# Kernel tuning notes

Hardware: AMD Instinct MI355X
Metric: run time of the kernel (lower is better)

Reference implementation:

```python
import jax, jax.numpy as jnp
import numpy as np

B, C, D, H, W = 8, 1, 128, 160, 128

def setup_inputs() -> dict:
    key = jax.random.key(0)
    kx, kb = jax.random.split(key)
    x = jax.random.normal(kx, (B, C, D, H, W), dtype=jnp.float32)
    base_volume = jax.random.normal(kb, (C, D, H, W), dtype=jnp.float32)
    return {"x": x, "base_volume": base_volume}

def reference(x, base_volume):
    # skimage match_histograms for continuous float images reduces (for a.e.-unique
    # values) to: map each source voxel's empirical CDF quantile onto the template's
    # inverse CDF via linear interpolation.
    tmpl = base_volume.ravel()
    t_sorted = jnp.sort(tmpl)                      # template inverse-CDF values
    M = tmpl.shape[0]
    tq = jnp.arange(1, M + 1, dtype=x.dtype) / M   # template CDF quantiles

    def match_one(sample):
        flat = sample.ravel()
        N = flat.shape[0]
        # rank of each voxel within its own sample (double argsort)
        ranks = jnp.argsort(jnp.argsort(flat))
        q = (ranks + 1).astype(flat.dtype) / N     # source empirical CDF
        matched = jnp.interp(q, tq, t_sorted)
        return matched.reshape(sample.shape)

    matched_vol = jax.vmap(match_one)(x)
    # self.model is identity here (the kernel headroom is the matching itself)
    return matched_vol
```

## Files before the change

kernel.cpp:

```cpp
#include <hip/hip_runtime.h>
#include <stdint.h>


#define SEG_N 2621440
#define NSEG 9
#define TILE 4096
#define NBLK (SEG_N / TILE)
#define RADIX 256
#define HL (RADIX * NBLK)
#define SCHUNK 4096
#define SNB (HL / SCHUNK)
#define SBUF (TILE + (TILE >> 4))

__device__ __forceinline__ uint32_t fkey(float f) {
  uint32_t b = __float_as_uint(f);
  return b ^ ((b & 0x80000000u) ? 0xFFFFFFFFu : 0x80000000u);
}
__device__ __forceinline__ float finv(uint32_t u) {
  uint32_t b = u ^ ((u & 0x80000000u) ? 0x80000000u : 0xFFFFFFFFu);
  return __uint_as_float(b);
}
__device__ __forceinline__ uint32_t SIDX(uint32_t i) { return i + (i >> 4); }

__global__ __launch_bounds__(256) void init_k(const float* __restrict__ x,
                                              const float* __restrict__ tmpl,
                                              int segbase,
                                              uint64_t* __restrict__ pairsA,
                                              uint32_t* __restrict__ Hkb) {
  __shared__ uint32_t hist[RADIX];
  const int t = threadIdx.x;
  const int blk = blockIdx.x;
  const int sl = blockIdx.y;
  const int seg = segbase + sl;
  const float* src = (seg == 0) ? tmpl : (x + (size_t)(seg - 1) * SEG_N);
  uint64_t* pa = pairsA + (size_t)sl * SEG_N;
  hist[t] = 0;
  __syncthreads();
  const uint32_t base = blk * TILE;
  const float4* s4 = reinterpret_cast<const float4*>(src + base);
#pragma unroll
  for (int r = 0; r < 4; ++r) {
    float4 v = s4[r * 256 + t];
    uint32_t i0 = base + (uint32_t)(r * 256 + t) * 4u;
    float f[4] = {v.x, v.y, v.z, v.w};
#pragma unroll
    for (int c = 0; c < 4; ++c) {
      uint32_t k = fkey(f[c]);
      atomicAdd(&hist[k & 255u], 1u);
      pa[i0 + c] = ((uint64_t)k << 32) | (uint64_t)(i0 + c);
    }
  }
  __syncthreads();
  Hkb[(size_t)sl * HL + (size_t)blk * RADIX + t] = hist[t];
}

__global__ __launch_bounds__(256) void hist_k(const uint64_t* __restrict__ pairs,
                                              uint32_t* __restrict__ Hkb, int p) {
  __shared__ uint32_t hist[RADIX];
  const int t = threadIdx.x;
  const int blk = blockIdx.x;
  const int sl = blockIdx.y;
  const uint64_t* pc = pairs + (size_t)sl * SEG_N + (size_t)blk * TILE;
  hist[t] = 0;
  __syncthreads();
  const int sh = 32 + 8 * p;
#pragma unroll
  for (int r = 0; r < 16; ++r) {
    uint64_t e = pc[r * 256 + t];
    atomicAdd(&hist[(uint32_t)(e >> sh) & 255u], 1u);
  }
  __syncthreads();
  Hkb[(size_t)sl * HL + (size_t)blk * RADIX + t] = hist[t];
}

__global__ __launch_bounds__(256) void transp_k(const uint32_t* __restrict__ Hkb,
                                                uint32_t* __restrict__ Hbk) {
  __shared__ uint32_t tile[64][65];
  const int sl = blockIdx.y;
  const uint32_t* src = Hkb + (size_t)sl * HL;
  uint32_t* dst = Hbk + (size_t)sl * HL;
  const int kt = blockIdx.x % (NBLK / 64);
  const int bt = blockIdx.x / (NBLK / 64);
  const int tx = threadIdx.x & 63, ty = threadIdx.x >> 6;
#pragma unroll
  for (int r = 0; r < 16; ++r) {
    int k = kt * 64 + ty + r * 4;
    tile[ty + r * 4][tx] = src[(size_t)k * RADIX + bt * 64 + tx];
  }
  __syncthreads();
#pragma unroll
  for (int r = 0; r < 16; ++r) {
    int b = bt * 64 + ty + r * 4;
    dst[(size_t)b * NBLK + kt * 64 + tx] = tile[tx][ty + r * 4];
  }
}

__device__ __forceinline__ uint32_t block_excl_scan_256(uint32_t v, uint32_t* lds) {
  const int t = threadIdx.x;
  lds[t] = v;
  __syncthreads();
#pragma unroll
  for (int off = 1; off < 256; off <<= 1) {
    uint32_t a = (t >= off) ? lds[t - off] : 0u;
    __syncthreads();
    lds[t] += a;
    __syncthreads();
  }
  uint32_t ex = (t == 0) ? 0u : lds[t - 1];
  __syncthreads();
  return ex;
}

__global__ __launch_bounds__(256) void scan_a_k(const uint32_t* __restrict__ Hbk,
                                                uint32_t* __restrict__ partials) {
  __shared__ uint32_t lds[256];
  const int t = threadIdx.x;
  const uint32_t* c = Hbk + (size_t)blockIdx.y * HL +
                      (size_t)blockIdx.x * SCHUNK + (size_t)t * 16;
  const uint4* p = reinterpret_cast<const uint4*>(c);
  uint32_t s = 0;
#pragma unroll
  for (int k = 0; k < 4; ++k) { uint4 a = p[k]; s += a.x + a.y + a.z + a.w; }
  lds[t] = s;
  __syncthreads();
  for (int off = 128; off > 0; off >>= 1) {
    if (t < off) lds[t] += lds[t + off];
    __syncthreads();
  }
  if (t == 0) partials[blockIdx.y * 64 + blockIdx.x] = lds[0];
}

__global__ __launch_bounds__(256) void scan_b_k(uint32_t* __restrict__ partials) {
  __shared__ uint32_t lds[256];
  const int t = threadIdx.x;
  uint32_t* p = partials + blockIdx.y * 64;
  uint32_t v = (t < SNB) ? p[t] : 0u;
  uint32_t ex = block_excl_scan_256(v, lds);
  if (t < SNB) p[t] = ex;
}

__global__ __launch_bounds__(256) void scan_c_k(uint32_t* __restrict__ Hbk,
                                                const uint32_t* __restrict__ partials) {
  __shared__ uint32_t lds[256];
  const int t = threadIdx.x;
  uint32_t* c = Hbk + (size_t)blockIdx.y * HL +
                (size_t)blockIdx.x * SCHUNK + (size_t)t * 16;
  uint4* p = reinterpret_cast<uint4*>(c);
  uint4 a[4];
  uint32_t s = 0;
#pragma unroll
  for (int k = 0; k < 4; ++k) {
    a[k] = p[k];
    s += a[k].x + a[k].y + a[k].z + a[k].w;
  }
  uint32_t ex = block_excl_scan_256(s, lds);
  uint32_t run = partials[blockIdx.y * 64 + blockIdx.x] + ex;
#pragma unroll
  for (int k = 0; k < 4; ++k) {
    uint4 o;
    o.x = run; run += a[k].x;
    o.y = run; run += a[k].y;
    o.z = run; run += a[k].z;
    o.w = run; run += a[k].w;
    p[k] = o;
  }
}

__device__ __forceinline__ void scan_pack2(uint32_t v0, uint32_t v1, uint32_t* s,
                                           uint32_t& ex0, uint32_t& ex1,
                                           uint32_t& tot0, uint32_t& tot1) {
  const int lane = threadIdx.x & 63, w = threadIdx.x >> 6;
  uint32_t a = v0, b = v1;
#pragma unroll
  for (int o = 1; o < 64; o <<= 1) {
    uint32_t na = __shfl_up(a, (unsigned)o, 64);
    uint32_t nb = __shfl_up(b, (unsigned)o, 64);
    if (lane >= o) { a += na; b += nb; }
  }
  if (lane == 63) { s[w] = a; s[4 + w] = b; }
  __syncthreads();
  if (threadIdx.x == 0) {
    uint32_t r0 = 0, r1 = 0;
#pragma unroll
    for (int i = 0; i < 4; ++i) {
      uint32_t q0 = s[i], q1 = s[4 + i];
      s[i] = r0; s[4 + i] = r1;
      r0 += q0; r1 += q1;
    }
    s[8] = r0; s[9] = r1;
  }
  __syncthreads();
  ex0 = a - v0 + s[w];
  ex1 = b - v1 + s[4 + w];
  tot0 = s[8]; tot1 = s[9];
  __syncthreads();
}

template <int P, int MODE>
__global__ __launch_bounds__(256) void part_k(const uint64_t* __restrict__ src,
                                              uint64_t* __restrict__ dst,
                                              const uint32_t* __restrict__ Hbk,
                                              float* __restrict__ tsorted,
                                              float* __restrict__ out,
                                              int segbase, int slbase) {
  __shared__ uint64_t buf[SBUF];
  __shared__ uint32_t ldsStart[RADIX];
  __shared__ uint32_t ldsBase[RADIX];
  __shared__ uint32_t scanS[12];
  const int t = threadIdx.x;
  const int blk = blockIdx.x;
  const int sl = slbase + blockIdx.y;
  const int seg = segbase + sl;
  const uint64_t* ps = src + (size_t)sl * SEG_N + (size_t)blk * TILE;

  ldsBase[t] = Hbk[(size_t)sl * HL + (size_t)t * NBLK + blk];

#pragma unroll
  for (int r = 0; r < 16; ++r) buf[SIDX(r * 256 + t)] = ps[r * 256 + t];
  __syncthreads();

  uint64_t e[16];
#pragma unroll
  for (int rnd = 0; rnd < 4; ++rnd) {
#pragma unroll
    for (int j = 0; j < 16; ++j) e[j] = buf[SIDX(t * 16 + j)];
    uint32_t cnt[4] = {0u, 0u, 0u, 0u};
#pragma unroll
    for (int j = 0; j < 16; ++j) {
      uint32_t d2 = (uint32_t)(e[j] >> (32 + 8 * P + 2 * rnd)) & 3u;
      cnt[d2]++;
    }
    uint32_t p0 = cnt[0] | (cnt[1] << 16);
    uint32_t p1 = cnt[2] | (cnt[3] << 16);
    uint32_t ex0, ex1, tot0, tot1;
    scan_pack2(p0, p1, scanS, ex0, ex1, tot0, tot1);
    uint32_t t0 = tot0 & 0xffffu, t1 = tot0 >> 16, t2 = tot1 & 0xffffu;
    uint32_t pos[4];
    pos[0] = (ex0 & 0xffffu);
    pos[1] = t0 + (ex0 >> 16);
    pos[2] = t0 + t1 + (ex1 & 0xffffu);
    pos[3] = t0 + t1 + t2 + (ex1 >> 16);
#pragma unroll
    for (int j = 0; j < 16; ++j) {
      uint32_t d2 = (uint32_t)(e[j] >> (32 + 8 * P + 2 * rnd)) & 3u;
      buf[SIDX(pos[d2]++)] = e[j];
    }
    __syncthreads();
  }

  const uint8_t* b8 = reinterpret_cast<const uint8_t*>(buf);
#pragma unroll
  for (int r = 0; r < 16; ++r) {
    uint32_t s = (uint32_t)(r * 256 + t);
    e[r] = buf[SIDX(s)];
    uint32_t d = (uint32_t)(e[r] >> (32 + 8 * P)) & 255u;
    uint32_t dp = (s == 0) ? 0x100u
                           : (uint32_t)b8[(size_t)SIDX(s - 1) * 8 + 4 + P];
    if (d != dp) ldsStart[d] = s;
  }
  __syncthreads();

#pragma unroll
  for (int r = 0; r < 16; ++r) {
    uint32_t s = (uint32_t)(r * 256 + t);
    uint64_t el = e[r];
    uint32_t d = (uint32_t)(el >> (32 + 8 * P)) & 255u;
    uint32_t dest = ldsBase[d] + s - ldsStart[d];
    if (MODE == 0) {
      dst[(size_t)sl * SEG_N + dest] = el;
    } else if (MODE == 1) {
      tsorted[dest] = finv((uint32_t)(el >> 32));
    } else {
      out[(size_t)(seg - 1) * SEG_N + (uint32_t)el] = tsorted[dest];
    }
  }
}

extern "C" void kernel_launch(void* const* d_in, const int* in_sizes, int n_in,
                              void* d_out, int out_size, void* d_ws, size_t ws_size,
                              hipStream_t stream) {
  const float* x = (const float*)d_in[0];
  const float* tmpl = (const float*)d_in[1];
  float* out = (float*)d_out;

  auto need = [](int nb) -> size_t {
    return (size_t)nb * ((size_t)SEG_N * 16 + (size_t)HL * 8 + 256) +
           (size_t)SEG_N * 4 + 8192;
  };
  const int nb = (ws_size >= need(9)) ? 9 : (ws_size >= need(3)) ? 3 : 1;

  uint8_t* w = (uint8_t*)d_ws;
  size_t off = 0;
  auto carve = [&](size_t bytes) -> void* {
    void* p = w + off;
    off = (off + bytes + 255) & ~(size_t)255;
    return p;
  };
  uint64_t* pairsA = (uint64_t*)carve((size_t)nb * SEG_N * 8);
  uint64_t* pairsB = (uint64_t*)carve((size_t)nb * SEG_N * 8);
  uint32_t* Hkb = (uint32_t*)carve((size_t)nb * HL * 4);
  uint32_t* Hbk = (uint32_t*)carve((size_t)nb * HL * 4);
  uint32_t* partials = (uint32_t*)carve((size_t)nb * 64 * 4);
  float* tsorted = (float*)carve((size_t)SEG_N * 4);

  for (int g = 0; g < NSEG; g += nb) {
    const dim3 gi(NBLK, nb);
    const dim3 gt(40, nb);
    const dim3 gs(SNB, nb);
    const dim3 g1(1, nb);

    auto scan_h = [&]() {
      transp_k<<<gt, 256, 0, stream>>>(Hkb, Hbk);
      scan_a_k<<<gs, 256, 0, stream>>>(Hbk, partials);
      scan_b_k<<<g1, 256, 0, stream>>>(partials);
      scan_c_k<<<gs, 256, 0, stream>>>(Hbk, partials);
    };

    init_k<<<gi, 256, 0, stream>>>(x, tmpl, g, pairsA, Hkb);
    scan_h();
    part_k<0, 0><<<gi, 256, 0, stream>>>(pairsA, pairsB, Hbk, tsorted, out, g, 0);
    hist_k<<<gi, 256, 0, stream>>>(pairsB, Hkb, 1);
    scan_h();
    part_k<1, 0><<<gi, 256, 0, stream>>>(pairsB, pairsA, Hbk, tsorted, out, g, 0);
    hist_k<<<gi, 256, 0, stream>>>(pairsA, Hkb, 2);
    scan_h();
    part_k<2, 0><<<gi, 256, 0, stream>>>(pairsA, pairsB, Hbk, tsorted, out, g, 0);
    hist_k<<<gi, 256, 0, stream>>>(pairsB, Hkb, 3);
    scan_h();
    if (g == 0) {
      part_k<3, 1><<<dim3(NBLK, 1), 256, 0, stream>>>(pairsB, pairsA, Hbk,
                                                      tsorted, out, g, 0);
      if (nb > 1)
        part_k<3, 2><<<dim3(NBLK, nb - 1), 256, 0, stream>>>(pairsB, pairsA, Hbk,
                                                             tsorted, out, g, 1);
    } else {
      part_k<3, 2><<<dim3(NBLK, nb), 256, 0, stream>>>(pairsB, pairsA, Hbk,
                                                       tsorted, out, g, 0);
    }
  }
}
```

Before: 1.133 ms.

## Fuse next-pass histogram into radix scatter via global atomics, drop hist and transpose

```diff
diff --git a/kernel.cpp b/kernel.cpp
--- a/kernel.cpp
+++ b/kernel.cpp
@@ -54,25 +54,6 @@
   Hkb[(size_t)sl * HL + (size_t)blk * RADIX + t] = hist[t];
 }
 
-__global__ __launch_bounds__(256) void hist_k(const uint64_t* __restrict__ pairs,
-                                              uint32_t* __restrict__ Hkb, int p) {
-  __shared__ uint32_t hist[RADIX];
-  const int t = threadIdx.x;
-  const int blk = blockIdx.x;
-  const int sl = blockIdx.y;
-  const uint64_t* pc = pairs + (size_t)sl * SEG_N + (size_t)blk * TILE;
-  hist[t] = 0;
-  __syncthreads();
-  const int sh = 32 + 8 * p;
-#pragma unroll
-  for (int r = 0; r < 16; ++r) {
-    uint64_t e = pc[r * 256 + t];
-    atomicAdd(&hist[(uint32_t)(e >> sh) & 255u], 1u);
-  }
-  __syncthreads();
-  Hkb[(size_t)sl * HL + (size_t)blk * RADIX + t] = hist[t];
-}
-
 __global__ __launch_bounds__(256) void transp_k(const uint32_t* __restrict__ Hkb,
                                                 uint32_t* __restrict__ Hbk) {
   __shared__ uint32_t tile[64][65];
@@ -111,16 +92,23 @@
   return ex;
 }
 
-__global__ __launch_bounds__(256) void scan_a_k(const uint32_t* __restrict__ Hbk,
-                                                uint32_t* __restrict__ partials) {
+__global__ __launch_bounds__(256) void scan_a_k(const uint32_t* __restrict__ cnt,
+                                                uint32_t* __restrict__ partials,
+                                                uint32_t* __restrict__ zbuf) {
   __shared__ uint32_t lds[256];
   const int t = threadIdx.x;
-  const uint32_t* c = Hbk + (size_t)blockIdx.y * HL +
-                      (size_t)blockIdx.x * SCHUNK + (size_t)t * 16;
-  const uint4* p = reinterpret_cast<const uint4*>(c);
+  const size_t boff = (size_t)blockIdx.y * HL + (size_t)blockIdx.x * SCHUNK +
+                      (size_t)t * 16;
+  const uint4* p = reinterpret_cast<const uint4*>(cnt + boff);
   uint32_t s = 0;
 #pragma unroll
   for (int k = 0; k < 4; ++k) { uint4 a = p[k]; s += a.x + a.y + a.z + a.w; }
+  if (zbuf) {
+    uint4* q = reinterpret_cast<uint4*>(zbuf + boff);
+    uint4 z = {0u, 0u, 0u, 0u};
+#pragma unroll
+    for (int k = 0; k < 4; ++k) q[k] = z;
+  }
   lds[t] = s;
   __syncthreads();
   for (int off = 128; off > 0; off >>= 1) {
@@ -139,11 +127,11 @@
   if (t < SNB) p[t] = ex;
 }
 
-__global__ __launch_bounds__(256) void scan_c_k(uint32_t* __restrict__ Hbk,
+__global__ __launch_bounds__(256) void scan_c_k(uint32_t* __restrict__ cnt,
                                                 const uint32_t* __restrict__ partials) {
   __shared__ uint32_t lds[256];
   const int t = threadIdx.x;
-  uint32_t* c = Hbk + (size_t)blockIdx.y * HL +
+  uint32_t* c = cnt + (size_t)blockIdx.y * HL +
                 (size_t)blockIdx.x * SCHUNK + (size_t)t * 16;
   uint4* p = reinterpret_cast<uint4*>(c);
   uint4 a[4];
@@ -196,10 +184,11 @@
   __syncthreads();
 }
 
-template <int P, int MODE>
+template <int P, int MODE, int ACC>
 __global__ __launch_bounds__(256) void part_k(const uint64_t* __restrict__ src,
                                               uint64_t* __restrict__ dst,
                                               const uint32_t* __restrict__ Hbk,
+                                              uint32_t* __restrict__ HbkN,
                                               float* __restrict__ tsorted,
                                               float* __restrict__ out,
                                               int segbase, int slbase) {
@@ -264,14 +253,19 @@
   for (int r = 0; r < 16; ++r) {
     uint32_t s = (uint32_t)(r * 256 + t);
     uint64_t el = e[r];
-    uint32_t d = (uint32_t)(el >> (32 + 8 * P)) & 255u;
+    uint32_t key = (uint32_t)(el >> 32);
+    uint32_t d = (key >> (8 * P)) & 255u;
     uint32_t dest = ldsBase[d] + s - ldsStart[d];
     if (MODE == 0) {
       dst[(size_t)sl * SEG_N + dest] = el;
     } else if (MODE == 1) {
-      tsorted[dest] = finv((uint32_t)(el >> 32));
+      tsorted[dest] = finv(key);
     } else {
       out[(size_t)(seg - 1) * SEG_N + (uint32_t)el] = tsorted[dest];
+    }
+    if (ACC) {
+      uint32_t nd = (key >> (8 * (P + 1 < 4 ? P + 1 : 0))) & 255u;
+      atomicAdd(&HbkN[(size_t)sl * HL + (size_t)nd * NBLK + (dest >> 12)], 1u);
     }
   }
 }
@@ -309,33 +303,34 @@
     const dim3 gs(SNB, nb);
     const dim3 g1(1, nb);
 
-    auto scan_h = [&]() {
-      transp_k<<<gt, 256, 0, stream>>>(Hkb, Hbk);
-      scan_a_k<<<gs, 256, 0, stream>>>(Hbk, partials);
+    auto scan_h = [&](uint32_t* cur, uint32_t* zb) {
+      scan_a_k<<<gs, 256, 0, stream>>>(cur, partials, zb);
       scan_b_k<<<g1, 256, 0, stream>>>(partials);
-      scan_c_k<<<gs, 256, 0, stream>>>(Hbk, partials);
+      scan_c_k<<<gs, 256, 0, stream>>>(cur, partials);
     };
 
     init_k<<<gi, 256, 0, stream>>>(x, tmpl, g, pairsA, Hkb);
-    scan_h();
-    part_k<0, 0><<<gi, 256, 0, stream>>>(pairsA, pairsB, Hbk, tsorted, out, g, 0);
-    hist_k<<<gi, 256, 0, stream>>>(pairsB, Hkb, 1);
-    scan_h();
-    part_k<1, 0><<<gi, 256, 0, stream>>>(pairsB, pairsA, Hbk, tsorted, out, g, 0);
-    hist_k<<<gi, 256, 0, stream>>>(pairsA, Hkb, 2);
-    scan_h();
-    part_k<2, 0><<<gi, 256, 0, stream>>>(pairsA, pairsB, Hbk, tsorted, out, g, 0);
-    hist_k<<<gi, 256, 0, stream>>>(pairsB, Hkb, 3);
-    scan_h();
+    transp_k<<<gt, 256, 0, stream>>>(Hkb, Hbk);
+    scan_h(Hbk, Hkb);
+    part_k<0, 0, 1><<<gi, 256, 0, stream>>>(pairsA, pairsB, Hbk, Hkb,
+                                            tsorted, out, g, 0);
+    scan_h(Hkb, Hbk);
+    part_k<1, 0, 1><<<gi, 256, 0, stream>>>(pairsB, pairsA, Hkb, Hbk,
+                                            tsorted, out, g, 0);
+    scan_h(Hbk, Hkb);
+    part_k<2, 0, 1><<<gi, 256, 0, stream>>>(pairsA, pairsB, Hbk, Hkb,
+                                            tsorted, out, g, 0);
+    scan_h(Hkb, nullptr);
     if (g == 0) {
-      part_k<3, 1><<<dim3(NBLK, 1), 256, 0, stream>>>(pairsB, pairsA, Hbk,
-                                                      tsorted, out, g, 0);
+      part_k<3, 1, 0><<<dim3(NBLK, 1), 256, 0, stream>>>(pairsB, pairsA, Hkb,
+                                                         nullptr, tsorted, out,
+                                                         g, 0);
       if (nb > 1)
-        part_k<3, 2><<<dim3(NBLK, nb - 1), 256, 0, stream>>>(pairsB, pairsA, Hbk,
-                                                             tsorted, out, g, 1);
+        part_k<3, 2, 0><<<dim3(NBLK, nb - 1), 256, 0, stream>>>(
+            pairsB, pairsA, Hkb, nullptr, tsorted, out, g, 1);
     } else {
-      part_k<3, 2><<<dim3(NBLK, nb), 256, 0, stream>>>(pairsB, pairsA, Hbk,
-                                                       tsorted, out, g, 0);
-    }
-  }
-}
+      part_k<3, 2, 0><<<dim3(NBLK, nb), 256, 0, stream>>>(
+          pairsB, pairsA, Hkb, nullptr, tsorted, out, g, 0);
+    }
+  }
+}
```

Result: slower. 4.457 ms (+293.3%).

## Split radix-sort key/index pairs into separate arrays and skip template indices

Applied to the files above, without the earlier changes.

```diff
diff --git a/kernel.cpp b/kernel.cpp
--- a/kernel.cpp
+++ b/kernel.cpp
@@ -10,7 +10,7 @@
 #define HL (RADIX * NBLK)
 #define SCHUNK 4096
 #define SNB (HL / SCHUNK)
-#define SBUF (TILE + (TILE >> 4))
+#define SBUFE (TILE + (TILE >> 4))
 
 __device__ __forceinline__ uint32_t fkey(float f) {
   uint32_t b = __float_as_uint(f);
@@ -25,52 +25,66 @@
 __global__ __launch_bounds__(256) void init_k(const float* __restrict__ x,
                                               const float* __restrict__ tmpl,
                                               int segbase,
-                                              uint64_t* __restrict__ pairsA,
+                                              uint32_t* __restrict__ keyA,
+                                              uint32_t* __restrict__ idxA,
                                               uint32_t* __restrict__ Hkb) {
-  __shared__ uint32_t hist[RADIX];
+  __shared__ uint32_t hw[4 * RADIX];
   const int t = threadIdx.x;
   const int blk = blockIdx.x;
   const int sl = blockIdx.y;
   const int seg = segbase + sl;
   const float* src = (seg == 0) ? tmpl : (x + (size_t)(seg - 1) * SEG_N);
-  uint64_t* pa = pairsA + (size_t)sl * SEG_N;
-  hist[t] = 0;
-  __syncthreads();
+  uint32_t* ka = keyA + (size_t)sl * SEG_N;
+  uint32_t* ia = idxA + (size_t)sl * SEG_N;
+  hw[t] = 0; hw[t + 256] = 0; hw[t + 512] = 0; hw[t + 768] = 0;
+  __syncthreads();
+  const int w = t >> 6;
   const uint32_t base = blk * TILE;
   const float4* s4 = reinterpret_cast<const float4*>(src + base);
 #pragma unroll
   for (int r = 0; r < 4; ++r) {
     float4 v = s4[r * 256 + t];
     uint32_t i0 = base + (uint32_t)(r * 256 + t) * 4u;
-    float f[4] = {v.x, v.y, v.z, v.w};
-#pragma unroll
-    for (int c = 0; c < 4; ++c) {
-      uint32_t k = fkey(f[c]);
-      atomicAdd(&hist[k & 255u], 1u);
-      pa[i0 + c] = ((uint64_t)k << 32) | (uint64_t)(i0 + c);
-    }
-  }
-  __syncthreads();
-  Hkb[(size_t)sl * HL + (size_t)blk * RADIX + t] = hist[t];
-}
-
-__global__ __launch_bounds__(256) void hist_k(const uint64_t* __restrict__ pairs,
+    uint4 kv;
+    kv.x = fkey(v.x); kv.y = fkey(v.y); kv.z = fkey(v.z); kv.w = fkey(v.w);
+    atomicAdd(&hw[w * 256 + (kv.x & 255u)], 1u);
+    atomicAdd(&hw[w * 256 + (kv.y & 255u)], 1u);
+    atomicAdd(&hw[w * 256 + (kv.z & 255u)], 1u);
+    atomicAdd(&hw[w * 256 + (kv.w & 255u)], 1u);
+    *reinterpret_cast<uint4*>(ka + i0) = kv;
+    if (seg != 0) {
+      uint4 iv = {i0, i0 + 1u, i0 + 2u, i0 + 3u};
+      *reinterpret_cast<uint4*>(ia + i0) = iv;
+    }
+  }
+  __syncthreads();
+  Hkb[(size_t)sl * HL + (size_t)blk * RADIX + t] =
+      hw[t] + hw[t + 256] + hw[t + 512] + hw[t + 768];
+}
+
+__global__ __launch_bounds__(256) void hist_k(const uint32_t* __restrict__ keys,
                                               uint32_t* __restrict__ Hkb, int p) {
-  __shared__ uint32_t hist[RADIX];
+  __shared__ uint32_t hw[4 * RADIX];
   const int t = threadIdx.x;
   const int blk = blockIdx.x;
   const int sl = blockIdx.y;
-  const uint64_t* pc = pairs + (size_t)sl * SEG_N + (size_t)blk * TILE;
-  hist[t] = 0;
-  __syncthreads();
-  const int sh = 32 + 8 * p;
-#pragma unroll
-  for (int r = 0; r < 16; ++r) {
-    uint64_t e = pc[r * 256 + t];
-    atomicAdd(&hist[(uint32_t)(e >> sh) & 255u], 1u);
-  }
-  __syncthreads();
-  Hkb[(size_t)sl * HL + (size_t)blk * RADIX + t] = hist[t];
+  const uint32_t* kc = keys + (size_t)sl * SEG_N + (size_t)blk * TILE;
+  hw[t] = 0; hw[t + 256] = 0; hw[t + 512] = 0; hw[t + 768] = 0;
+  __syncthreads();
+  const int w = t >> 6;
+  const int sh = 8 * p;
+  const uint4* k4 = reinterpret_cast<const uint4*>(kc);
+#pragma unroll
+  for (int r = 0; r < 4; ++r) {
+    uint4 v = k4[r * 256 + t];
+    atomicAdd(&hw[w * 256 + ((v.x >> sh) & 255u)], 1u);
+    atomicAdd(&hw[w * 256 + ((v.y >> sh) & 255u)], 1u);
+    atomicAdd(&hw[w * 256 + ((v.z >> sh) & 255u)], 1u);
+    atomicAdd(&hw[w * 256 + ((v.w >> sh) & 255u)], 1u);
+  }
+  __syncthreads();
+  Hkb[(size_t)sl * HL + (size_t)blk * RADIX + t] =
+      hw[t] + hw[t + 256] + hw[t + 512] + hw[t + 768];
 }
 
 __global__ __launch_bounds__(256) void transp_k(const uint32_t* __restrict__ Hkb,
@@ -197,13 +211,16 @@
 }
 
 template <int P, int MODE>
-__global__ __launch_bounds__(256) void part_k(const uint64_t* __restrict__ src,
-                                              uint64_t* __restrict__ dst,
+__global__ __launch_bounds__(256) void part_k(const uint32_t* __restrict__ keyIn,
+                                              const uint32_t* __restrict__ idxIn,
+                                              uint32_t* __restrict__ keyOut,
+                                              uint32_t* __restrict__ idxOut,
                                               const uint32_t* __restrict__ Hbk,
                                               float* __restrict__ tsorted,
                                               float* __restrict__ out,
                                               int segbase, int slbase) {
-  __shared__ uint64_t buf[SBUF];
+  __shared__ uint32_t bufK[SBUFE];
+  __shared__ uint16_t bufP[SBUFE];
   __shared__ uint32_t ldsStart[RADIX];
   __shared__ uint32_t ldsBase[RADIX];
   __shared__ uint32_t scanS[12];
@@ -211,23 +228,34 @@
   const int blk = blockIdx.x;
   const int sl = slbase + blockIdx.y;
   const int seg = segbase + sl;
-  const uint64_t* ps = src + (size_t)sl * SEG_N + (size_t)blk * TILE;
+  const bool wantIdx = (seg != 0);
+  const size_t segOff = (size_t)sl * SEG_N;
+  const uint32_t blkBase = (uint32_t)blk * TILE;
+  const uint32_t* ks = keyIn + segOff + blkBase;
 
   ldsBase[t] = Hbk[(size_t)sl * HL + (size_t)t * NBLK + blk];
 
 #pragma unroll
-  for (int r = 0; r < 16; ++r) buf[SIDX(r * 256 + t)] = ps[r * 256 + t];
-  __syncthreads();
-
-  uint64_t e[16];
+  for (int r = 0; r < 16; ++r) {
+    uint32_t s = (uint32_t)(r * 256 + t);
+    bufK[SIDX(s)] = ks[s];
+    bufP[SIDX(s)] = (uint16_t)s;
+  }
+  __syncthreads();
+
+  uint32_t k[16];
+  uint16_t pr[16];
 #pragma unroll
   for (int rnd = 0; rnd < 4; ++rnd) {
 #pragma unroll
-    for (int j = 0; j < 16; ++j) e[j] = buf[SIDX(t * 16 + j)];
+    for (int j = 0; j < 16; ++j) {
+      k[j] = bufK[SIDX(t * 16 + j)];
+      pr[j] = bufP[SIDX(t * 16 + j)];
+    }
     uint32_t cnt[4] = {0u, 0u, 0u, 0u};
 #pragma unroll
     for (int j = 0; j < 16; ++j) {
-      uint32_t d2 = (uint32_t)(e[j] >> (32 + 8 * P + 2 * rnd)) & 3u;
+      uint32_t d2 = (k[j] >> (8 * P + 2 * rnd)) & 3u;
       cnt[d2]++;
     }
     uint32_t p0 = cnt[0] | (cnt[1] << 16);
@@ -242,20 +270,23 @@
     pos[3] = t0 + t1 + t2 + (ex1 >> 16);
 #pragma unroll
     for (int j = 0; j < 16; ++j) {
-      uint32_t d2 = (uint32_t)(e[j] >> (32 + 8 * P + 2 * rnd)) & 3u;
-      buf[SIDX(pos[d2]++)] = e[j];
+      uint32_t d2 = (k[j] >> (8 * P + 2 * rnd)) & 3u;
+      uint32_t pp = pos[d2]++;
+      bufK[SIDX(pp)] = k[j];
+      bufP[SIDX(pp)] = pr[j];
     }
     __syncthreads();
   }
 
-  const uint8_t* b8 = reinterpret_cast<const uint8_t*>(buf);
+  const uint8_t* b8 = reinterpret_cast<const uint8_t*>(bufK);
 #pragma unroll
   for (int r = 0; r < 16; ++r) {
     uint32_t s = (uint32_t)(r * 256 + t);
-    e[r] = buf[SIDX(s)];
-    uint32_t d = (uint32_t)(e[r] >> (32 + 8 * P)) & 255u;
+    k[r] = bufK[SIDX(s)];
+    pr[r] = bufP[SIDX(s)];
+    uint32_t d = (k[r] >> (8 * P)) & 255u;
     uint32_t dp = (s == 0) ? 0x100u
-                           : (uint32_t)b8[(size_t)SIDX(s - 1) * 8 + 4 + P];
+                           : (uint32_t)b8[(size_t)SIDX(s - 1) * 4 + P];
     if (d != dp) ldsStart[d] = s;
   }
   __syncthreads();
@@ -263,15 +294,17 @@
 #pragma unroll
   for (int r = 0; r < 16; ++r) {
     uint32_t s = (uint32_t)(r * 256 + t);
-    uint64_t el = e[r];
-    uint32_t d = (uint32_t)(el >> (32 + 8 * P)) & 255u;
+    uint32_t key = k[r];
+    uint32_t d = (key >> (8 * P)) & 255u;
     uint32_t dest = ldsBase[d] + s - ldsStart[d];
     if (MODE == 0) {
-      dst[(size_t)sl * SEG_N + dest] = el;
+      keyOut[segOff + dest] = key;
+      if (wantIdx) idxOut[segOff + dest] = idxIn[segOff + blkBase + pr[r]];
     } else if (MODE == 1) {
-      tsorted[dest] = finv((uint32_t)(el >> 32));
+      tsorted[dest] = finv(key);
     } else {
-      out[(size_t)(seg - 1) * SEG_N + (uint32_t)el] = tsorted[dest];
+      uint32_t gidx = idxIn[segOff + blkBase + pr[r]];
+      out[(size_t)(seg - 1) * SEG_N + gidx] = tsorted[dest];
     }
   }
 }
@@ -296,8 +329,10 @@
     off = (off + bytes + 255) & ~(size_t)255;
     return p;
   };
-  uint64_t* pairsA = (uint64_t*)carve((size_t)nb * SEG_N * 8);
-  uint64_t* pairsB = (uint64_t*)carve((size_t)nb * SEG_N * 8);
+  uint32_t* keyA = (uint32_t*)carve((size_t)nb * SEG_N * 4);
+  uint32_t* keyB = (uint32_t*)carve((size_t)nb * SEG_N * 4);
+  uint32_t* idxA = (uint32_t*)carve((size_t)nb * SEG_N * 4);
+  uint32_t* idxB = (uint32_t*)carve((size_t)nb * SEG_N * 4);
   uint32_t* Hkb = (uint32_t*)carve((size_t)nb * HL * 4);
   uint32_t* Hbk = (uint32_t*)carve((size_t)nb * HL * 4);
   uint32_t* partials = (uint32_t*)carve((size_t)nb * 64 * 4);
@@ -316,26 +351,29 @@
       scan_c_k<<<gs, 256, 0, stream>>>(Hbk, partials);
     };
 
-    init_k<<<gi, 256, 0, stream>>>(x, tmpl, g, pairsA, Hkb);
+    init_k<<<gi, 256, 0, stream>>>(x, tmpl, g, keyA, idxA, Hkb);
     scan_h();
-    part_k<0, 0><<<gi, 256, 0, stream>>>(pairsA, pairsB, Hbk, tsorted, out, g, 0);
-    hist_k<<<gi, 256, 0, stream>>>(pairsB, Hkb, 1);
+    part_k<0, 0><<<gi, 256, 0, stream>>>(keyA, idxA, keyB, idxB, Hbk,
+                                         tsorted, out, g, 0);
+    hist_k<<<gi, 256, 0, stream>>>(keyB, Hkb, 1);
     scan_h();
-    part_k<1, 0><<<gi, 256, 0, stream>>>(pairsB, pairsA, Hbk, tsorted, out, g, 0);
-    hist_k<<<gi, 256, 0, stream>>>(pairsA, Hkb, 2);
+    part_k<1, 0><<<gi, 256, 0, stream>>>(keyB, idxB, keyA, idxA, Hbk,
+                                         tsorted, out, g, 0);
+    hist_k<<<gi, 256, 0, stream>>>(keyA, Hkb, 2);
     scan_h();
-    part_k<2, 0><<<gi, 256, 0, stream>>>(pairsA, pairsB, Hbk, tsorted, out, g, 0);
-    hist_k<<<gi, 256, 0, stream>>>(pairsB, Hkb, 3);
+    part_k<2, 0><<<gi, 256, 0, stream>>>(keyA, idxA, keyB, idxB, Hbk,
+                                         tsorted, out, g, 0);
+    hist_k<<<gi, 256, 0, stream>>>(keyB, Hkb, 3);
     scan_h();
     if (g == 0) {
-      part_k<3, 1><<<dim3(NBLK, 1), 256, 0, stream>>>(pairsB, pairsA, Hbk,
-                                                      tsorted, out, g, 0);
+      part_k<3, 1><<<dim3(NBLK, 1), 256, 0, stream>>>(keyB, idxB, keyA, idxA,
+                                                      Hbk, tsorted, out, g, 0);
       if (nb > 1)
-        part_k<3, 2><<<dim3(NBLK, nb - 1), 256, 0, stream>>>(pairsB, pairsA, Hbk,
-                                                             tsorted, out, g, 1);
+        part_k<3, 2><<<dim3(NBLK, nb - 1), 256, 0, stream>>>(
+            keyB, idxB, keyA, idxA, Hbk, tsorted, out, g, 1);
     } else {
-      part_k<3, 2><<<dim3(NBLK, nb), 256, 0, stream>>>(pairsB, pairsA, Hbk,
-                                                       tsorted, out, g, 0);
-    }
-  }
-}
+      part_k<3, 2><<<dim3(NBLK, nb), 256, 0, stream>>>(
+          keyB, idxB, keyA, idxA, Hbk, tsorted, out, g, 0);
+    }
+  }
+}
```

Result: slower. 1.171 ms (+3.3%).

## Fuse histogram transpose and scan into single decoupled-lookback kernel, 4-bit local split

Applied to the files above, without the earlier changes.

```diff
diff --git a/kernel.cpp b/kernel.cpp
--- a/kernel.cpp
+++ b/kernel.cpp
@@ -27,15 +27,16 @@
                                               int segbase,
                                               uint64_t* __restrict__ pairsA,
                                               uint32_t* __restrict__ Hkb) {
-  __shared__ uint32_t hist[RADIX];
+  __shared__ uint32_t hw[4 * RADIX];
   const int t = threadIdx.x;
   const int blk = blockIdx.x;
   const int sl = blockIdx.y;
   const int seg = segbase + sl;
   const float* src = (seg == 0) ? tmpl : (x + (size_t)(seg - 1) * SEG_N);
   uint64_t* pa = pairsA + (size_t)sl * SEG_N;
-  hist[t] = 0;
-  __syncthreads();
+  hw[t] = 0; hw[t + 256] = 0; hw[t + 512] = 0; hw[t + 768] = 0;
+  __syncthreads();
+  const int w = t >> 6;
   const uint32_t base = blk * TILE;
   const float4* s4 = reinterpret_cast<const float4*>(src + base);
 #pragma unroll
@@ -46,58 +47,58 @@
 #pragma unroll
     for (int c = 0; c < 4; ++c) {
       uint32_t k = fkey(f[c]);
-      atomicAdd(&hist[k & 255u], 1u);
+      atomicAdd(&hw[w * 256 + (k & 255u)], 1u);
       pa[i0 + c] = ((uint64_t)k << 32) | (uint64_t)(i0 + c);
     }
   }
   __syncthreads();
-  Hkb[(size_t)sl * HL + (size_t)blk * RADIX + t] = hist[t];
+  Hkb[(size_t)sl * HL + (size_t)blk * RADIX + t] =
+      hw[t] + hw[t + 256] + hw[t + 512] + hw[t + 768];
 }
 
 __global__ __launch_bounds__(256) void hist_k(const uint64_t* __restrict__ pairs,
                                               uint32_t* __restrict__ Hkb, int p) {
-  __shared__ uint32_t hist[RADIX];
+  __shared__ uint32_t hw[4 * RADIX];
   const int t = threadIdx.x;
   const int blk = blockIdx.x;
   const int sl = blockIdx.y;
-  const uint64_t* pc = pairs + (size_t)sl * SEG_N + (size_t)blk * TILE;
-  hist[t] = 0;
-  __syncthreads();
+  hw[t] = 0; hw[t + 256] = 0; hw[t + 512] = 0; hw[t + 768] = 0;
+  __syncthreads();
+  const int w = t >> 6;
   const int sh = 32 + 8 * p;
-#pragma unroll
-  for (int r = 0; r < 16; ++r) {
-    uint64_t e = pc[r * 256 + t];
-    atomicAdd(&hist[(uint32_t)(e >> sh) & 255u], 1u);
-  }
-  __syncthreads();
-  Hkb[(size_t)sl * HL + (size_t)blk * RADIX + t] = hist[t];
-}
-
-__global__ __launch_bounds__(256) void transp_k(const uint32_t* __restrict__ Hkb,
-                                                uint32_t* __restrict__ Hbk) {
-  __shared__ uint32_t tile[64][65];
+  const ulonglong2* pc = reinterpret_cast<const ulonglong2*>(
+      pairs + (size_t)sl * SEG_N + (size_t)blk * TILE);
+#pragma unroll
+  for (int r = 0; r < 8; ++r) {
+    ulonglong2 v = pc[r * 256 + t];
+    atomicAdd(&hw[w * 256 + ((uint32_t)(v.x >> sh) & 255u)], 1u);
+    atomicAdd(&hw[w * 256 + ((uint32_t)(v.y >> sh) & 255u)], 1u);
+  }
+  __syncthreads();
+  Hkb[(size_t)sl * HL + (size_t)blk * RADIX + t] =
+      hw[t] + hw[t + 256] + hw[t + 512] + hw[t + 768];
+}
+
+__global__ __launch_bounds__(256) void scanT_k(const uint32_t* __restrict__ Hkb,
+                                               uint32_t* __restrict__ Hbk,
+                                               uint32_t* __restrict__ desc) {
+  __shared__ uint32_t lds[256];
+  __shared__ uint32_t baseS;
+  const int t = threadIdx.x;
+  const int c = blockIdx.x;
   const int sl = blockIdx.y;
   const uint32_t* src = Hkb + (size_t)sl * HL;
-  uint32_t* dst = Hbk + (size_t)sl * HL;
-  const int kt = blockIdx.x % (NBLK / 64);
-  const int bt = blockIdx.x / (NBLK / 64);
-  const int tx = threadIdx.x & 63, ty = threadIdx.x >> 6;
-#pragma unroll
-  for (int r = 0; r < 16; ++r) {
-    int k = kt * 64 + ty + r * 4;
-    tile[ty + r * 4][tx] = src[(size_t)k * RADIX + bt * 64 + tx];
-  }
-  __syncthreads();
-#pragma unroll
-  for (int r = 0; r < 16; ++r) {
-    int b = bt * 64 + ty + r * 4;
-    dst[(size_t)b * NBLK + kt * 64 + tx] = tile[tx][ty + r * 4];
-  }
-}
-
-__device__ __forceinline__ uint32_t block_excl_scan_256(uint32_t v, uint32_t* lds) {
-  const int t = threadIdx.x;
-  lds[t] = v;
+  const uint32_t e0 = (uint32_t)c * SCHUNK + (uint32_t)t * 16;
+  uint32_t vals[16];
+  uint32_t s = 0;
+#pragma unroll
+  for (int i = 0; i < 16; ++i) {
+    uint32_t e = e0 + (uint32_t)i;
+    uint32_t bin = e / NBLK, blk = e - bin * NBLK;
+    vals[i] = src[(size_t)blk * RADIX + bin];
+    s += vals[i];
+  }
+  lds[t] = s;
   __syncthreads();
 #pragma unroll
   for (int off = 1; off < 256; off <<= 1) {
@@ -106,94 +107,41 @@
     lds[t] += a;
     __syncthreads();
   }
-  uint32_t ex = (t == 0) ? 0u : lds[t - 1];
-  __syncthreads();
-  return ex;
-}
-
-__global__ __launch_bounds__(256) void scan_a_k(const uint32_t* __restrict__ Hbk,
-                                                uint32_t* __restrict__ partials) {
-  __shared__ uint32_t lds[256];
-  const int t = threadIdx.x;
-  const uint32_t* c = Hbk + (size_t)blockIdx.y * HL +
-                      (size_t)blockIdx.x * SCHUNK + (size_t)t * 16;
-  const uint4* p = reinterpret_cast<const uint4*>(c);
-  uint32_t s = 0;
-#pragma unroll
-  for (int k = 0; k < 4; ++k) { uint4 a = p[k]; s += a.x + a.y + a.z + a.w; }
-  lds[t] = s;
-  __syncthreads();
-  for (int off = 128; off > 0; off >>= 1) {
-    if (t < off) lds[t] += lds[t + off];
-    __syncthreads();
-  }
-  if (t == 0) partials[blockIdx.y * 64 + blockIdx.x] = lds[0];
-}
-
-__global__ __launch_bounds__(256) void scan_b_k(uint32_t* __restrict__ partials) {
-  __shared__ uint32_t lds[256];
-  const int t = threadIdx.x;
-  uint32_t* p = partials + blockIdx.y * 64;
-  uint32_t v = (t < SNB) ? p[t] : 0u;
-  uint32_t ex = block_excl_scan_256(v, lds);
-  if (t < SNB) p[t] = ex;
-}
-
-__global__ __launch_bounds__(256) void scan_c_k(uint32_t* __restrict__ Hbk,
-                                                const uint32_t* __restrict__ partials) {
-  __shared__ uint32_t lds[256];
-  const int t = threadIdx.x;
-  uint32_t* c = Hbk + (size_t)blockIdx.y * HL +
-                (size_t)blockIdx.x * SCHUNK + (size_t)t * 16;
-  uint4* p = reinterpret_cast<uint4*>(c);
-  uint4 a[4];
-  uint32_t s = 0;
-#pragma unroll
-  for (int k = 0; k < 4; ++k) {
-    a[k] = p[k];
-    s += a[k].x + a[k].y + a[k].z + a[k].w;
-  }
-  uint32_t ex = block_excl_scan_256(s, lds);
-  uint32_t run = partials[blockIdx.y * 64 + blockIdx.x] + ex;
-#pragma unroll
-  for (int k = 0; k < 4; ++k) {
-    uint4 o;
-    o.x = run; run += a[k].x;
-    o.y = run; run += a[k].y;
-    o.z = run; run += a[k].z;
-    o.w = run; run += a[k].w;
-    p[k] = o;
-  }
-}
-
-__device__ __forceinline__ void scan_pack2(uint32_t v0, uint32_t v1, uint32_t* s,
-                                           uint32_t& ex0, uint32_t& ex1,
-                                           uint32_t& tot0, uint32_t& tot1) {
-  const int lane = threadIdx.x & 63, w = threadIdx.x >> 6;
-  uint32_t a = v0, b = v1;
-#pragma unroll
-  for (int o = 1; o < 64; o <<= 1) {
-    uint32_t na = __shfl_up(a, (unsigned)o, 64);
-    uint32_t nb = __shfl_up(b, (unsigned)o, 64);
-    if (lane >= o) { a += na; b += nb; }
-  }
-  if (lane == 63) { s[w] = a; s[4 + w] = b; }
-  __syncthreads();
-  if (threadIdx.x == 0) {
-    uint32_t r0 = 0, r1 = 0;
-#pragma unroll
-    for (int i = 0; i < 4; ++i) {
-      uint32_t q0 = s[i], q1 = s[4 + i];
-      s[i] = r0; s[4 + i] = r1;
-      r0 += q0; r1 += q1;
-    }
-    s[8] = r0; s[9] = r1;
-  }
-  __syncthreads();
-  ex0 = a - v0 + s[w];
-  ex1 = b - v1 + s[4 + w];
-  tot0 = s[8]; tot1 = s[9];
-  __syncthreads();
+  const uint32_t incl = lds[t];
+  const uint32_t total = lds[255];
+  const uint32_t ex = incl - s;
+
+  uint32_t* dseg = desc + sl * SNB;
+  if (t == 0) {
+    __hip_atomic_store(&dseg[c], (total & 0x3FFFFFFFu) |
+                                     ((c == 0 ? 2u : 1u) << 30),
+                       __ATOMIC_RELAXED, __HIP_MEMORY_SCOPE_AGENT);
+    uint32_t acc = 0;
+    if (c > 0) {
+      int b = c - 1;
+      for (;;) {
+        uint32_t v;
+        do {
+          v = __hip_atomic_load(&dseg[b], __ATOMIC_RELAXED,
+                                __HIP_MEMORY_SCOPE_AGENT);
+        } while ((v >> 30) == 0u);
+        acc += v & 0x3FFFFFFFu;
+        if ((v >> 30) == 2u) break;
+        --b;
+      }
+      __hip_atomic_store(&dseg[c], ((acc + total) & 0x3FFFFFFFu) | (2u << 30),
+                         __ATOMIC_RELAXED, __HIP_MEMORY_SCOPE_AGENT);
+    }
+    baseS = acc;
+  }
+  __syncthreads();
+  uint32_t run = baseS + ex;
+  uint32_t* dst = Hbk + (size_t)sl * HL + e0;
+#pragma unroll
+  for (int i = 0; i < 16; ++i) {
+    dst[i] = run;
+    run += vals[i];
+  }
 }
 
 template <int P, int MODE>
@@ -206,7 +154,7 @@
   __shared__ uint64_t buf[SBUF];
   __shared__ uint32_t ldsStart[RADIX];
   __shared__ uint32_t ldsBase[RADIX];
-  __shared__ uint32_t scanS[12];
+  __shared__ uint32_t scanS[48];
   const int t = threadIdx.x;
   const int blk = blockIdx.x;
   const int sl = slbase + blockIdx.y;
@@ -220,30 +168,75 @@
   __syncthreads();
 
   uint64_t e[16];
-#pragma unroll
-  for (int rnd = 0; rnd < 4; ++rnd) {
+  const int lane = t & 63, w = t >> 6;
+#pragma unroll
+  for (int rnd = 0; rnd < 2; ++rnd) {
+    const int sh = 32 + 8 * P + 4 * rnd;
 #pragma unroll
     for (int j = 0; j < 16; ++j) e[j] = buf[SIDX(t * 16 + j)];
-    uint32_t cnt[4] = {0u, 0u, 0u, 0u};
+    uint32_t cntW[4] = {0u, 0u, 0u, 0u};
 #pragma unroll
     for (int j = 0; j < 16; ++j) {
-      uint32_t d2 = (uint32_t)(e[j] >> (32 + 8 * P + 2 * rnd)) & 3u;
-      cnt[d2]++;
-    }
-    uint32_t p0 = cnt[0] | (cnt[1] << 16);
-    uint32_t p1 = cnt[2] | (cnt[3] << 16);
-    uint32_t ex0, ex1, tot0, tot1;
-    scan_pack2(p0, p1, scanS, ex0, ex1, tot0, tot1);
-    uint32_t t0 = tot0 & 0xffffu, t1 = tot0 >> 16, t2 = tot1 & 0xffffu;
-    uint32_t pos[4];
-    pos[0] = (ex0 & 0xffffu);
-    pos[1] = t0 + (ex0 >> 16);
-    pos[2] = t0 + t1 + (ex1 & 0xffffu);
-    pos[3] = t0 + t1 + t2 + (ex1 >> 16);
+      uint32_t d4 = (uint32_t)(e[j] >> sh) & 15u;
+      cntW[d4 >> 2] += 1u << ((d4 & 3u) * 8u);
+    }
+    uint32_t v[8], a[8];
+#pragma unroll
+    for (int q = 0; q < 8; ++q) {
+      uint32_t word = cntW[q >> 1];
+      uint32_t s2 = (q & 1) * 16;
+      v[q] = ((word >> s2) & 0xffu) | (((word >> (s2 + 8)) & 0xffu) << 16);
+      a[q] = v[q];
+    }
+#pragma unroll
+    for (int o = 1; o < 64; o <<= 1) {
+#pragma unroll
+      for (int q = 0; q < 8; ++q) {
+        uint32_t n = __shfl_up(a[q], (unsigned)o, 64);
+        if (lane >= o) a[q] += n;
+      }
+    }
+    if (lane == 63) {
+#pragma unroll
+      for (int q = 0; q < 8; ++q) scanS[w * 8 + q] = a[q];
+    }
+    __syncthreads();
+    if (t == 0) {
+      uint32_t run = 0;
+#pragma unroll
+      for (int q = 0; q < 8; ++q) {
+        uint32_t r0 = 0;
+#pragma unroll
+        for (int ww = 0; ww < 4; ++ww) {
+          uint32_t xv = scanS[ww * 8 + q];
+          scanS[ww * 8 + q] = r0;
+          r0 += xv;
+        }
+        uint32_t b0 = r0 & 0xffffu, b1 = r0 >> 16;
+        scanS[32 + q] = run | ((run + b0) << 16);
+        run += b0 + b1;
+      }
+    }
+    __syncthreads();
+    uint64_t posW[4];
+#pragma unroll
+    for (int q = 0; q < 8; ++q) {
+      uint32_t exq = a[q] - v[q] + scanS[w * 8 + q];
+      uint32_t base = scanS[32 + q];
+      uint32_t p0 = (base & 0xffffu) + (exq & 0xffffu);
+      uint32_t p1 = (base >> 16) + (exq >> 16);
+      uint64_t pk = (uint64_t)p0 | ((uint64_t)p1 << 16);
+      if ((q & 1) == 0) posW[q >> 1] = pk;
+      else posW[q >> 1] |= pk << 32;
+    }
 #pragma unroll
     for (int j = 0; j < 16; ++j) {
-      uint32_t d2 = (uint32_t)(e[j] >> (32 + 8 * P + 2 * rnd)) & 3u;
-      buf[SIDX(pos[d2]++)] = e[j];
+      uint32_t d4 = (uint32_t)(e[j] >> sh) & 15u;
+      uint32_t hi = d4 >> 2;
+      uint32_t fs = (d4 & 3u) * 16u;
+      uint32_t p = (uint32_t)(posW[hi] >> fs) & 0xffffu;
+      posW[hi] += (uint64_t)1 << fs;
+      buf[SIDX(p)] = e[j];
     }
     __syncthreads();
   }
@@ -264,12 +257,13 @@
   for (int r = 0; r < 16; ++r) {
     uint32_t s = (uint32_t)(r * 256 + t);
     uint64_t el = e[r];
-    uint32_t d = (uint32_t)(el >> (32 + 8 * P)) & 255u;
+    uint32_t key = (uint32_t)(el >> 32);
+    uint32_t d = (key >> (8 * P)) & 255u;
     uint32_t dest = ldsBase[d] + s - ldsStart[d];
     if (MODE == 0) {
       dst[(size_t)sl * SEG_N + dest] = el;
     } else if (MODE == 1) {
-      tsorted[dest] = finv((uint32_t)(el >> 32));
+      tsorted[dest] = finv(key);
     } else {
       out[(size_t)(seg - 1) * SEG_N + (uint32_t)el] = tsorted[dest];
     }
@@ -284,8 +278,8 @@
   float* out = (float*)d_out;
 
   auto need = [](int nb) -> size_t {
-    return (size_t)nb * ((size_t)SEG_N * 16 + (size_t)HL * 8 + 256) +
-           (size_t)SEG_N * 4 + 8192;
+    return (size_t)nb * ((size_t)SEG_N * 16 + (size_t)HL * 8 + 4096) +
+           (size_t)SEG_N * 4 + 16384;
   };
   const int nb = (ws_size >= need(9)) ? 9 : (ws_size >= need(3)) ? 3 : 1;
 
@@ -300,33 +294,26 @@
   uint64_t* pairsB = (uint64_t*)carve((size_t)nb * SEG_N * 8);
   uint32_t* Hkb = (uint32_t*)carve((size_t)nb * HL * 4);
   uint32_t* Hbk = (uint32_t*)carve((size_t)nb * HL * 4);
-  uint32_t* partials = (uint32_t*)carve((size_t)nb * 64 * 4);
+  uint32_t* desc = (uint32_t*)carve((size_t)4 * nb * SNB * 4);
   float* tsorted = (float*)carve((size_t)SEG_N * 4);
 
   for (int g = 0; g < NSEG; g += nb) {
     const dim3 gi(NBLK, nb);
-    const dim3 gt(40, nb);
     const dim3 gs(SNB, nb);
-    const dim3 g1(1, nb);
-
-    auto scan_h = [&]() {
-      transp_k<<<gt, 256, 0, stream>>>(Hkb, Hbk);
-      scan_a_k<<<gs, 256, 0, stream>>>(Hbk, partials);
-      scan_b_k<<<g1, 256, 0, stream>>>(partials);
-      scan_c_k<<<gs, 256, 0, stream>>>(Hbk, partials);
-    };
+
+    hipMemsetAsync(desc, 0, (size_t)4 * nb * SNB * 4, stream);
 
     init_k<<<gi, 256, 0, stream>>>(x, tmpl, g, pairsA, Hkb);
-    scan_h();
+    scanT_k<<<gs, 256, 0, stream>>>(Hkb, Hbk, desc + 0 * nb * SNB);
     part_k<0, 0><<<gi, 256, 0, stream>>>(pairsA, pairsB, Hbk, tsorted, out, g, 0);
     hist_k<<<gi, 256, 0, stream>>>(pairsB, Hkb, 1);
-    scan_h();
+    scanT_k<<<gs, 256, 0, stream>>>(Hkb, Hbk, desc + 1 * nb * SNB);
     part_k<1, 0><<<gi, 256, 0, stream>>>(pairsB, pairsA, Hbk, tsorted, out, g, 0);
     hist_k<<<gi, 256, 0, stream>>>(pairsA, Hkb, 2);
-    scan_h();
+    scanT_k<<<gs, 256, 0, stream>>>(Hkb, Hbk, desc + 2 * nb * SNB);
     part_k<2, 0><<<gi, 256, 0, stream>>>(pairsA, pairsB, Hbk, tsorted, out, g, 0);
     hist_k<<<gi, 256, 0, stream>>>(pairsB, Hkb, 3);
-    scan_h();
+    scanT_k<<<gs, 256, 0, stream>>>(Hkb, Hbk, desc + 3 * nb * SNB);
     if (g == 0) {
       part_k<3, 1><<<dim3(NBLK, 1), 256, 0, stream>>>(pairsB, pairsA, Hbk,
                                                       tsorted, out, g, 0);
```

Measured after the change: 1.162 ms. +2.6%, slower.
